# Optimization experiments

Measured on AMD Instinct MI355X. Metric: run time of the kernel, lower is better.

The kernel has to match this reference:

```python
import jax, jax.numpy as jnp
import numpy as np


def setup_inputs() -> dict:
    key = jax.random.key(0)
    ks = jax.random.split(key, 7)
    T, K, D_x, D_y = 8192, 64, 128, 64
    X = jax.random.normal(ks[0], (T, D_x), dtype=jnp.float32)
    Y = jax.random.normal(ks[1], (T, D_y), dtype=jnp.float32)
    # learned parameters (small random values for non-degenerate math)
    init_logits = jax.random.normal(ks[2], (K,), dtype=jnp.float32) * 0.1
    W = jax.random.normal(ks[3], (K, K, D_x), dtype=jnp.float32) * 0.05
    b = jax.random.normal(ks[4], (K, K), dtype=jnp.float32) * 0.1
    mu = jax.random.normal(ks[5], (K, D_y), dtype=jnp.float32) * 0.1
    log_var_unconstrained = jax.random.normal(ks[6], (K, D_y), dtype=jnp.float32) * 0.1
    return {"X": X, "Y": Y, "init_logits": init_logits, "W": W, "b": b,
            "mu": mu, "log_var_unconstrained": log_var_unconstrained}


def reference(X, Y, init_logits, W, b, mu, log_var_unconstrained):
    # log pi0
    log_pi0 = jax.nn.log_softmax(init_logits)
    # emissions for all t: diagonal Gaussian log-pdf, log_em [T, K]
    log_var = jnp.clip(log_var_unconstrained, -6.0, 6.0)  # [K, D_y]
    D = Y.shape[-1]
    LOG2PI = jnp.log(jnp.asarray(2.0 * np.pi, dtype=Y.dtype))
    diff = Y[:, None, :] - mu[None, :, :]                 # [T, K, D_y]
    quad = jnp.sum(diff * diff * jnp.exp(-log_var)[None], axis=-1)  # [T, K]
    logdet = jnp.sum(log_var, axis=-1)                    # [K]
    log_em = -0.5 * (D * LOG2PI + logdet[None, :] + quad)  # [T, K]
    # time-varying transition logits: b_ij + x_t . W_ij, row-softmax over j
    logits = b[None, :, :] + jnp.einsum('ijd,td->tij', W, X)  # [T, K, K]
    log_A = jax.nn.log_softmax(logits, axis=2)                 # [T, K, K]
    # forward recursion: alpha_t(j) = log_em_t(j) + logsumexp_i(alpha_{t-1}(i) + log_A_t(i,j))
    alpha0 = log_pi0 + log_em[0]

    def step(alpha, inputs):
        log_A_t, log_em_t = inputs
        alpha_new = log_em_t + jax.nn.logsumexp(alpha[:, None] + log_A_t, axis=0)
        return alpha_new, None

    alpha_T, _ = jax.lax.scan(step, alpha0, (log_A[1:], log_em[1:]))
    loglik = jax.nn.logsumexp(alpha_T)
    return loglik
```

## Files before the change

### kernel.cpp

```cpp
#include <hip/hip_runtime.h>
#include <hip/hip_bf16.h>


typedef unsigned int u32;
typedef unsigned short u16;

#define T_LEN 8192

typedef __attribute__((ext_vector_type(8))) short bf16x8;
typedef __attribute__((ext_vector_type(4))) float f32x4;

__device__ __forceinline__ float bflo(u32 u){ return __uint_as_float(u << 16); }
__device__ __forceinline__ float bfhi(u32 u){ return __uint_as_float(u & 0xffff0000u); }
__device__ __forceinline__ u32 f2bf(float x){
  u32 b = __float_as_uint(x);
  return (b + 0x7fffu + ((b >> 16) & 1u)) >> 16;
}
__device__ __forceinline__ u32 pack2bf(float a, float b){
  return f2bf(a) | (f2bf(b) << 16);
}

__global__ __launch_bounds__(64) void k_prep(
    const float* __restrict__ mu, const float* __restrict__ lvu,
    float* __restrict__ muT, float* __restrict__ ivT, float* __restrict__ logdet)
{
  const int k = threadIdx.x;
  float ld = 0.f;
  for (int d = 0; d < 64; ++d){
    float lv = fminf(fmaxf(lvu[k*64 + d], -6.f), 6.f);
    ld += lv;
    muT[d*64 + k] = mu[k*64 + d];
    ivT[d*64 + k] = __expf(-lv);
  }
  logdet[k] = ld;
}

__global__ __launch_bounds__(256) void k_emis(
    const float* __restrict__ Y, const float* __restrict__ muT,
    const float* __restrict__ ivT, const float* __restrict__ logdet,
    float* __restrict__ emp, float* __restrict__ cvec)
{
  const int w = threadIdx.x >> 6, k = threadIdx.x & 63;
  const int t = blockIdx.x * 4 + w;
  float y = Y[(size_t)t*64 + k];
  float quad = 0.f;
  #pragma unroll 8
  for (int d = 0; d < 64; ++d){
    float yd = __shfl(y, d, 64);
    float df = yd - muT[d*64 + k];
    quad = fmaf(df*df, ivT[d*64 + k], quad);
  }
  float le = -0.5f*(117.6241322f + logdet[k] + quad);
  float m = le;
  #pragma unroll
  for (int off = 1; off < 64; off <<= 1) m = fmaxf(m, __shfl_xor(m, off, 64));
  emp[(size_t)t*64 + k] = __expf(le - m);
  if (k == 0) cvec[t] = m;
}

__global__ __launch_bounds__(256) void k_trans(
    const float* __restrict__ X, const float* __restrict__ W,
    const float* __restrict__ bmat, const float* __restrict__ emp,
    u16* __restrict__ Ap)
{
  __shared__ __align__(16) u16 Xs[128*128];
  __shared__ __align__(16) u16 Ws[64*128];
  const int tid = threadIdx.x;
  const int t0 = blockIdx.x * 128;
  const int i  = blockIdx.y;

  {
    const float4* xs = (const float4*)(X + (size_t)t0 * 128);
    #pragma unroll
    for (int u = 0; u < 16; ++u){
      int f = u*256 + tid;
      float4 v = xs[f];
      int row = f >> 5, c = f & 31;
      int byte = (row*256 + c*8) ^ ((row & 7) << 4);
      *(uint2*)((char*)Xs + byte) = make_uint2(pack2bf(v.x, v.y), pack2bf(v.z, v.w));
    }
    const float4* wsrc = (const float4*)(W + (size_t)i * 8192);
    #pragma unroll
    for (int u = 0; u < 8; ++u){
      int f = u*256 + tid;
      float4 v = wsrc[f];
      int row = f >> 5, c = f & 31;
      int byte = (row*256 + c*8) ^ ((row & 7) << 4);
      *(uint2*)((char*)Ws + byte) = make_uint2(pack2bf(v.x, v.y), pack2bf(v.z, v.w));
    }
  }
  __syncthreads();

  const int lane = tid & 63, w = tid >> 6;
  const int lr = lane & 15, lg = lane >> 4;

  f32x4 acc[2][4] = {};
  #pragma unroll
  for (int kg = 0; kg < 4; ++kg){
    const int kbyte = kg*64 + lg*16;
    bf16x8 a[2], b[4];
    #pragma unroll
    for (int mt = 0; mt < 2; ++mt){
      int row = w*32 + mt*16 + lr;
      a[mt] = *(const bf16x8*)((const char*)Xs + ((row*256 + kbyte) ^ ((row&7)<<4)));
    }
    #pragma unroll
    for (int nt = 0; nt < 4; ++nt){
      int row = nt*16 + lr;
      b[nt] = *(const bf16x8*)((const char*)Ws + ((row*256 + kbyte) ^ ((row&7)<<4)));
    }
    #pragma unroll
    for (int mt = 0; mt < 2; ++mt)
      #pragma unroll
      for (int nt = 0; nt < 4; ++nt)
        acc[mt][nt] = __builtin_amdgcn_mfma_f32_16x16x32_bf16(a[mt], b[nt], acc[mt][nt], 0, 0, 0);
  }

  float bv[4];
  #pragma unroll
  for (int nt = 0; nt < 4; ++nt) bv[nt] = bmat[i*64 + nt*16 + lr];

  __syncthreads();
  u16* Ct = Xs;

  #pragma unroll
  for (int mt = 0; mt < 2; ++mt){
    #pragma unroll
    for (int reg = 0; reg < 4; ++reg){
      const int row = w*32 + mt*16 + lg*4 + reg;
      const int t = t0 + row;
      float v0 = acc[mt][0][reg] + bv[0];
      float v1 = acc[mt][1][reg] + bv[1];
      float v2 = acc[mt][2][reg] + bv[2];
      float v3 = acc[mt][3][reg] + bv[3];
      float mx = fmaxf(fmaxf(v0,v1), fmaxf(v2,v3));
      #pragma unroll
      for (int off = 1; off < 16; off <<= 1) mx = fmaxf(mx, __shfl_xor(mx, off, 64));
      float e0 = __expf(v0-mx), e1 = __expf(v1-mx), e2 = __expf(v2-mx), e3 = __expf(v3-mx);
      float sum = e0 + e1 + e2 + e3;
      #pragma unroll
      for (int off = 1; off < 16; off <<= 1) sum += __shfl_xor(sum, off, 64);
      float inv = 1.0f / sum;
      const float* er = emp + (size_t)t*64;
      const int sw = (row & 7) << 4;
      *(u16*)((char*)Ct + row*128 + ((( 0 + lr)*2) ^ sw)) = (u16)f2bf(e0*inv*er[ 0 + lr]);
      *(u16*)((char*)Ct + row*128 + (((16 + lr)*2) ^ sw)) = (u16)f2bf(e1*inv*er[16 + lr]);
      *(u16*)((char*)Ct + row*128 + (((32 + lr)*2) ^ sw)) = (u16)f2bf(e2*inv*er[32 + lr]);
      *(u16*)((char*)Ct + row*128 + (((48 + lr)*2) ^ sw)) = (u16)f2bf(e3*inv*er[48 + lr]);
    }
  }
  __syncthreads();
  #pragma unroll
  for (int q = 0; q < 4; ++q){
    const int f = tid*4 + q;
    const int row = f >> 3, c = f & 7;
    uint4 v = *(const uint4*)((const char*)Ct + row*128 + ((c*16) ^ ((row & 7) << 4)));
    *(uint4*)(Ap + (size_t)(t0 + row)*4096 + (size_t)i*64 + c*8) = v;
  }
}

__global__ __launch_bounds__(256) void k_scan(
    u16* mats, int mstride, int per_wg, int skip0,
    const float* __restrict__ in_sc, float* __restrict__ out_sc)
{
  __shared__ u32 Apk[2][32*68];
  const int tid = threadIdx.x;
  const int lane = tid & 63, w = tid >> 6;
  const int r16 = lane & 15, oct = lane >> 4;
  int c0 = blockIdx.x * per_wg, cnt = per_wg;
  const size_t out_slot = (size_t)c0 * mstride;
  if (blockIdx.x == 0){ c0 += skip0; cnt -= skip0; }

  bf16x8 Bf[2];
  {
    const u16* m0 = mats + ((size_t)c0*mstride << 12) + (w*16 + r16)*64 + oct*8;
    Bf[0] = *(const bf16x8*)(m0);
    Bf[1] = *(const bf16x8*)(m0 + 32);
  }
  float S = in_sc ? in_sc[c0*4 + w] : 0.0f;

  const int lp = tid >> 3, c8 = tid & 7;
  auto STAGE = [&](int buf, const u16* src){
    const uint4 A = *(const uint4*)(src + lp*128 + c8*8);
    const uint4 B = *(const uint4*)(src + lp*128 + 64 + c8*8);
    uint4 o0, o1;
    o0.x = (A.x & 0xffffu) | (B.x << 16);
    o0.y = (A.x >> 16)     | (B.x & 0xffff0000u);
    o0.z = (A.y & 0xffffu) | (B.y << 16);
    o0.w = (A.y >> 16)     | (B.y & 0xffff0000u);
    o1.x = (A.z & 0xffffu) | (B.z << 16);
    o1.y = (A.z >> 16)     | (B.z & 0xffff0000u);
    o1.z = (A.w & 0xffffu) | (B.w << 16);
    o1.w = (A.w >> 16)     | (B.w & 0xffff0000u);
    u32* dst = &Apk[buf][lp*68 + c8*8];
    *(uint4*)(dst)     = o0;
    *(uint4*)(dst + 4) = o1;
  };

  if (cnt > 1) STAGE(0, mats + ((size_t)(c0+1)*mstride << 12));
  __syncthreads();
  int cur = 0;
  for (int kk = 1; kk < cnt; ++kk){
    if (kk + 1 < cnt) STAGE(cur ^ 1, mats + ((size_t)(c0 + kk + 1)*mstride << 12));

    if (in_sc){
      const float* sp = in_sc + (size_t)(c0 + kk)*4;
      float s0=sp[0], s1=sp[1], s2=sp[2], s3=sp[3];
      float sm = fmaxf(fmaxf(s0,s1), fmaxf(s2,s3));
      S += sm;
      #pragma unroll
      for (int kt = 0; kt < 2; ++kt){
        float slo = (kt == 0) ? s0 : s2;
        float shi = (kt == 0) ? s1 : s3;
        float se = __expf(((oct >> 1) ? shi : slo) - sm);
        uint4 bv4 = __builtin_bit_cast(uint4, Bf[kt]);
        bv4.x = pack2bf(bflo(bv4.x)*se, bfhi(bv4.x)*se);
        bv4.y = pack2bf(bflo(bv4.y)*se, bfhi(bv4.y)*se);
        bv4.z = pack2bf(bflo(bv4.z)*se, bfhi(bv4.z)*se);
        bv4.w = pack2bf(bflo(bv4.w)*se, bfhi(bv4.w)*se);
        Bf[kt] = __builtin_bit_cast(bf16x8, bv4);
      }
    }

    f32x4 acc[4] = {};
    const u32* Ab = &Apk[cur][0];
    #pragma unroll
    for (int kt = 0; kt < 2; ++kt){
      const u32* gb = Ab + (kt*16 + oct*4)*68 + r16;
      #pragma unroll
      for (int jt = 0; jt < 4; ++jt){
        const u32* g = gb + jt*16;
        uint4 av = make_uint4(g[0], g[68], g[136], g[204]);
        acc[jt] = __builtin_amdgcn_mfma_f32_16x16x32_bf16(
            __builtin_bit_cast(bf16x8, av), Bf[kt], acc[jt], 0, 0, 0);
      }
    }

    float mx = acc[0][0];
    #pragma unroll
    for (int jt = 0; jt < 4; ++jt)
      #pragma unroll
      for (int q = 0; q < 4; ++q) mx = fmaxf(mx, acc[jt][q]);
    #pragma unroll
    for (int off = 1; off < 64; off <<= 1) mx = fmaxf(mx, __shfl_xor(mx, off, 64));
    float inv = 1.0f / mx;
    S += __logf(mx);

    u32 p0[4], p1[4];
    #pragma unroll
    for (int jt = 0; jt < 4; ++jt){
      p0[jt] = pack2bf(acc[jt][0]*inv, acc[jt][1]*inv);
      p1[jt] = pack2bf(acc[jt][2]*inv, acc[jt][3]*inv);
    }
    const int s0l = r16 + 32*(oct & 1), s1l = s0l + 16;
    const bool hi = (oct >> 1) != 0;
    #pragma unroll
    for (int kt = 0; kt < 2; ++kt){
      u32 a0 = __shfl(p0[2*kt],   s0l, 64), a1 = __shfl(p1[2*kt],   s0l, 64);
      u32 a2 = __shfl(p0[2*kt],   s1l, 64), a3 = __shfl(p1[2*kt],   s1l, 64);
      u32 b0 = __shfl(p0[2*kt+1], s0l, 64), b1 = __shfl(p1[2*kt+1], s0l, 64);
      u32 b2 = __shfl(p0[2*kt+1], s1l, 64), b3 = __shfl(p1[2*kt+1], s1l, 64);
      uint4 nb;
      nb.x = hi ? b0 : a0;
      nb.y = hi ? b1 : a1;
      nb.z = hi ? b2 : a2;
      nb.w = hi ? b3 : a3;
      Bf[kt] = __builtin_bit_cast(bf16x8, nb);
    }
    cur ^= 1;
    __syncthreads();
  }
  {
    u16* outp = mats + (out_slot << 12) + (w*16 + r16)*64 + oct*8;
    *(bf16x8*)(outp)      = Bf[0];
    *(bf16x8*)(outp + 32) = Bf[1];
    if (lane == 0) out_sc[blockIdx.x*4 + w] = S;
  }
}

__global__ __launch_bounds__(256) void k_final(
    const float* __restrict__ init_logits, const float* __restrict__ emp,
    const float* __restrict__ cvec, const u16* __restrict__ Mfin, int mstride,
    const float* __restrict__ scfin, int nmat, float* __restrict__ out)
{
  __shared__ float wsum[4];
  const int tid = threadIdx.x;
  float part = 0.f;
  for (int t = tid; t < T_LEN; t += 256) part += cvec[t];
  #pragma unroll
  for (int off = 1; off < 64; off <<= 1) part += __shfl_xor(part, off, 64);
  if ((tid & 63) == 0) wsum[tid >> 6] = part;
  __syncthreads();
  if (tid >= 64) return;
  const float csum = wsum[0] + wsum[1] + wsum[2] + wsum[3];
  const int k = tid;
  float ilv = init_logits[k];
  float m = ilv;
  #pragma unroll
  for (int off = 1; off < 64; off <<= 1) m = fmaxf(m, __shfl_xor(m, off, 64));
  float e = __expf(ilv - m);
  float s = e;
  #pragma unroll
  for (int off = 1; off < 64; off <<= 1) s += __shfl_xor(s, off, 64);
  float alpha = (e / s) * emp[k];
  float S = 0.f;
  for (int d = 0; d < nmat; ++d){
    const float* sp = scfin + d*4;
    float sm = fmaxf(fmaxf(sp[0], sp[1]), fmaxf(sp[2], sp[3]));
    alpha *= __expf(sp[k >> 4] - sm);
    S += sm;
    const u16* Mp = Mfin + ((size_t)d*mstride << 12);
    float an = 0.f;
    for (int i2 = 0; i2 < 64; ++i2){
      float av = __shfl(alpha, i2, 64);
      an = fmaf(av, __uint_as_float(((u32)Mp[i2*64 + k]) << 16), an);
    }
    float mx = an;
    #pragma unroll
    for (int off = 1; off < 64; off <<= 1) mx = fmaxf(mx, __shfl_xor(mx, off, 64));
    alpha = an / mx;
    S += __logf(mx);
  }
  float tot = alpha;
  #pragma unroll
  for (int off = 1; off < 64; off <<= 1) tot += __shfl_xor(tot, off, 64);
  if (k == 0) out[0] = __logf(tot) + S + csum;
}

extern "C" void kernel_launch(void* const* d_in, const int* in_sizes, int n_in,
                              void* d_out, int out_size, void* d_ws, size_t ws_size,
                              hipStream_t stream)
{
  const float* X  = (const float*)d_in[0];
  const float* Y  = (const float*)d_in[1];
  const float* il = (const float*)d_in[2];
  const float* W  = (const float*)d_in[3];
  const float* bm = (const float*)d_in[4];
  const float* mu = (const float*)d_in[5];
  const float* lv = (const float*)d_in[6];
  float* out = (float*)d_out;
  char* ws = (char*)d_ws;
  (void)in_sizes; (void)n_in; (void)out_size; (void)ws_size;

  float* emp    = (float*)(ws + 0x0000000);
  float* cvec   = (float*)(ws + 0x0200000);
  float* muT    = (float*)(ws + 0x0210000);
  float* ivT    = (float*)(ws + 0x0214000);
  float* logdet = (float*)(ws + 0x0218000);
  float* sc1    = (float*)(ws + 0x0220000);
  float* sc2    = (float*)(ws + 0x0224000);
  float* sc3    = (float*)(ws + 0x0225000);
  float* sc4    = (float*)(ws + 0x0226000);
  float* sc5    = (float*)(ws + 0x0227000);
  u16*   Ap     = (u16*)  (ws + 0x0400000);

  k_prep <<<1, 64, 0, stream>>>(mu, lv, muT, ivT, logdet);
  k_emis <<<2048, 256, 0, stream>>>(Y, muT, ivT, logdet, emp, cvec);
  k_trans<<<dim3(64, 64), 256, 0, stream>>>(X, W, bm, emp, Ap);
  k_scan <<<1024, 256, 0, stream>>>(Ap,   1, 8, 1, (const float*)nullptr, sc1);
  k_scan <<<256,  256, 0, stream>>>(Ap,   8, 4, 0, sc1, sc2);
  k_scan <<<64,   256, 0, stream>>>(Ap,  32, 4, 0, sc2, sc3);
  k_scan <<<16,   256, 0, stream>>>(Ap, 128, 4, 0, sc3, sc4);
  k_scan <<<4,    256, 0, stream>>>(Ap, 512, 4, 0, sc4, sc5);
  k_final<<<1, 256, 0, stream>>>(il, emp, cvec, Ap, 2048, sc5, 4, out);
}
```

Baseline: 196.2 us.

## Pre-convert X/W to swizzled bf16, restructure transition GEMM and scan tree

X and W are converted once to swizzled bf16 inside the emission kernel, so the transition kernel can load tiles straight into LDS with global_load_lds and skip repeated fp32 conversion. The transition GEMM is retiled to 64 timesteps by 2 source states per block, with W rows as the MFMA A operand. The softmax drops the max subtraction and reduces row sums through shared memory. The scan tree goes from five levels to four with wider per-block fan-in. Skipping the max subtraction could overflow for large logits, and the wider scan levels reduce parallelism at each level.

Result: slower. 205.2 us (+4.6%).

```diff
diff --git a/kernel.cpp b/kernel.cpp
--- a/kernel.cpp
+++ b/kernel.cpp
@@ -18,6 +18,16 @@
 }
 __device__ __forceinline__ u32 pack2bf(float a, float b){
   return f2bf(a) | (f2bf(b) << 16);
+}
+
+__device__ __forceinline__ void gld_lds16(const void* g, void* l){
+#if defined(__has_builtin) && __has_builtin(__builtin_amdgcn_global_load_lds)
+  __builtin_amdgcn_global_load_lds(
+      (const __attribute__((address_space(1))) unsigned int*)g,
+      (__attribute__((address_space(3))) unsigned int*)l, 16, 0, 0);
+#else
+  *(uint4*)((char*)l + (threadIdx.x & 63) * 16) = *(const uint4*)g;
+#endif
 }
 
 __global__ __launch_bounds__(64) void k_prep(
@@ -38,9 +48,12 @@
 __global__ __launch_bounds__(256) void k_emis(
     const float* __restrict__ Y, const float* __restrict__ muT,
     const float* __restrict__ ivT, const float* __restrict__ logdet,
-    float* __restrict__ emp, float* __restrict__ cvec)
-{
-  const int w = threadIdx.x >> 6, k = threadIdx.x & 63;
+    const float* __restrict__ X, const float* __restrict__ W,
+    float* __restrict__ emp, float* __restrict__ cvec,
+    u16* __restrict__ Xsw, u16* __restrict__ Wsw)
+{
+  const int tid = threadIdx.x;
+  const int w = tid >> 6, k = tid & 63;
   const int t = blockIdx.x * 4 + w;
   float y = Y[(size_t)t*64 + k];
   float quad = 0.f;
@@ -56,106 +69,138 @@
   for (int off = 1; off < 64; off <<= 1) m = fmaxf(m, __shfl_xor(m, off, 64));
   emp[(size_t)t*64 + k] = __expf(le - m);
   if (k == 0) cvec[t] = m;
+
+  if (tid < 128){
+    int rl = tid >> 5, c32 = tid & 31;
+    int tr = blockIdx.x*4 + rl;
+    float4 v = *(const float4*)(X + (size_t)tr*128 + c32*4);
+    int c16 = c32 >> 1, h = c32 & 1;
+    int byte = tr*256 + ((c16 ^ (tr & 7))*16 + h*8);
+    *(uint2*)((char*)Xsw + byte) = make_uint2(pack2bf(v.x,v.y), pack2bf(v.z,v.w));
+  }
+  if (blockIdx.x < 512){
+    int f4 = blockIdx.x*256 + tid;
+    int r = f4 >> 5, c32 = f4 & 31;
+    float4 v = *(const float4*)(W + (size_t)f4*4);
+    int c16 = c32 >> 1, h = c32 & 1;
+    int byte = r*256 + ((c16 ^ (r & 7))*16 + h*8);
+    *(uint2*)((char*)Wsw + byte) = make_uint2(pack2bf(v.x,v.y), pack2bf(v.z,v.w));
+  }
 }
 
 __global__ __launch_bounds__(256) void k_trans(
-    const float* __restrict__ X, const float* __restrict__ W,
+    const u16* __restrict__ Xsw, const u16* __restrict__ Wsw,
     const float* __restrict__ bmat, const float* __restrict__ emp,
     u16* __restrict__ Ap)
 {
-  __shared__ __align__(16) u16 Xs[128*128];
-  __shared__ __align__(16) u16 Ws[64*128];
+  __shared__ __align__(16) u16 Wt[128*128];
+  __shared__ __align__(16) u16 Xt[64*128];
+  __shared__ float Sred[8][64];
   const int tid = threadIdx.x;
-  const int t0 = blockIdx.x * 128;
-  const int i  = blockIdx.y;
-
-  {
-    const float4* xs = (const float4*)(X + (size_t)t0 * 128);
-    #pragma unroll
-    for (int u = 0; u < 16; ++u){
-      int f = u*256 + tid;
-      float4 v = xs[f];
-      int row = f >> 5, c = f & 31;
-      int byte = (row*256 + c*8) ^ ((row & 7) << 4);
-      *(uint2*)((char*)Xs + byte) = make_uint2(pack2bf(v.x, v.y), pack2bf(v.z, v.w));
-    }
-    const float4* wsrc = (const float4*)(W + (size_t)i * 8192);
-    #pragma unroll
-    for (int u = 0; u < 8; ++u){
-      int f = u*256 + tid;
-      float4 v = wsrc[f];
-      int row = f >> 5, c = f & 31;
-      int byte = (row*256 + c*8) ^ ((row & 7) << 4);
-      *(uint2*)((char*)Ws + byte) = make_uint2(pack2bf(v.x, v.y), pack2bf(v.z, v.w));
-    }
-  }
-  __syncthreads();
-
   const int lane = tid & 63, w = tid >> 6;
   const int lr = lane & 15, lg = lane >> 4;
+  const int t0 = blockIdx.x * 64;
+  const int i0 = blockIdx.y * 2;
+
+  {
+    const char* xsrc = (const char*)(Xsw + (size_t)t0*128);
+    const char* wsrc = (const char*)(Wsw + (size_t)i0*64*128);
+    #pragma unroll
+    for (int c = 0; c < 4; ++c){
+      int kb = w*4 + c;
+      gld_lds16(xsrc + kb*1024 + lane*16, (char*)Xt + kb*1024);
+    }
+    #pragma unroll
+    for (int c = 0; c < 8; ++c){
+      int kb = w*8 + c;
+      gld_lds16(wsrc + kb*1024 + lane*16, (char*)Wt + kb*1024);
+    }
+  }
+  __syncthreads();
 
   f32x4 acc[2][4] = {};
   #pragma unroll
   for (int kg = 0; kg < 4; ++kg){
-    const int kbyte = kg*64 + lg*16;
+    const int kc = kg*4 + lg;
     bf16x8 a[2], b[4];
     #pragma unroll
-    for (int mt = 0; mt < 2; ++mt){
-      int row = w*32 + mt*16 + lr;
-      a[mt] = *(const bf16x8*)((const char*)Xs + ((row*256 + kbyte) ^ ((row&7)<<4)));
-    }
-    #pragma unroll
-    for (int nt = 0; nt < 4; ++nt){
-      int row = nt*16 + lr;
-      b[nt] = *(const bf16x8*)((const char*)Ws + ((row*256 + kbyte) ^ ((row&7)<<4)));
-    }
-    #pragma unroll
-    for (int mt = 0; mt < 2; ++mt)
+    for (int jt = 0; jt < 2; ++jt){
+      int row = (w + jt*4)*16 + lr;
+      a[jt] = *(const bf16x8*)((const char*)Wt + row*256 + ((kc ^ (row & 7))*16));
+    }
+    #pragma unroll
+    for (int tt = 0; tt < 4; ++tt){
+      int row = tt*16 + lr;
+      b[tt] = *(const bf16x8*)((const char*)Xt + row*256 + ((kc ^ (row & 7))*16));
+    }
+    #pragma unroll
+    for (int jt = 0; jt < 2; ++jt)
       #pragma unroll
-      for (int nt = 0; nt < 4; ++nt)
-        acc[mt][nt] = __builtin_amdgcn_mfma_f32_16x16x32_bf16(a[mt], b[nt], acc[mt][nt], 0, 0, 0);
-  }
-
-  float bv[4];
-  #pragma unroll
-  for (int nt = 0; nt < 4; ++nt) bv[nt] = bmat[i*64 + nt*16 + lr];
+      for (int tt = 0; tt < 4; ++tt)
+        acc[jt][tt] = __builtin_amdgcn_mfma_f32_16x16x32_bf16(a[jt], b[tt], acc[jt][tt], 0, 0, 0);
+  }
+
+  float bvv[2][4];
+  #pragma unroll
+  for (int jt = 0; jt < 2; ++jt){
+    int q = w + jt*4;
+    int ig = i0 + (q >> 2);
+    #pragma unroll
+    for (int reg = 0; reg < 4; ++reg)
+      bvv[jt][reg] = bmat[ig*64 + (q & 3)*16 + lg*4 + reg];
+  }
 
   __syncthreads();
-  u16* Ct = Xs;
-
-  #pragma unroll
-  for (int mt = 0; mt < 2; ++mt){
-    #pragma unroll
-    for (int reg = 0; reg < 4; ++reg){
-      const int row = w*32 + mt*16 + lg*4 + reg;
-      const int t = t0 + row;
-      float v0 = acc[mt][0][reg] + bv[0];
-      float v1 = acc[mt][1][reg] + bv[1];
-      float v2 = acc[mt][2][reg] + bv[2];
-      float v3 = acc[mt][3][reg] + bv[3];
-      float mx = fmaxf(fmaxf(v0,v1), fmaxf(v2,v3));
-      #pragma unroll
-      for (int off = 1; off < 16; off <<= 1) mx = fmaxf(mx, __shfl_xor(mx, off, 64));
-      float e0 = __expf(v0-mx), e1 = __expf(v1-mx), e2 = __expf(v2-mx), e3 = __expf(v3-mx);
-      float sum = e0 + e1 + e2 + e3;
-      #pragma unroll
-      for (int off = 1; off < 16; off <<= 1) sum += __shfl_xor(sum, off, 64);
-      float inv = 1.0f / sum;
-      const float* er = emp + (size_t)t*64;
-      const int sw = (row & 7) << 4;
-      *(u16*)((char*)Ct + row*128 + ((( 0 + lr)*2) ^ sw)) = (u16)f2bf(e0*inv*er[ 0 + lr]);
-      *(u16*)((char*)Ct + row*128 + (((16 + lr)*2) ^ sw)) = (u16)f2bf(e1*inv*er[16 + lr]);
-      *(u16*)((char*)Ct + row*128 + (((32 + lr)*2) ^ sw)) = (u16)f2bf(e2*inv*er[32 + lr]);
-      *(u16*)((char*)Ct + row*128 + (((48 + lr)*2) ^ sw)) = (u16)f2bf(e3*inv*er[48 + lr]);
+  u16* Ct = Xt;
+
+  #pragma unroll
+  for (int jt = 0; jt < 2; ++jt){
+    const int q = w + jt*4;
+    #pragma unroll
+    for (int tt = 0; tt < 4; ++tt){
+      const int t = tt*16 + lr;
+      float e0 = __expf(acc[jt][tt][0] + bvv[jt][0]);
+      float e1 = __expf(acc[jt][tt][1] + bvv[jt][1]);
+      float e2 = __expf(acc[jt][tt][2] + bvv[jt][2]);
+      float e3 = __expf(acc[jt][tt][3] + bvv[jt][3]);
+      float s = e0 + e1 + e2 + e3;
+      s += __shfl_xor(s, 16, 64);
+      s += __shfl_xor(s, 32, 64);
+      if (lg == 0) Sred[q][t] = s;
+      const int byte = t*256 + ((q*32 + lg*8) ^ ((t & 7) << 4));
+      *(u32*)((char*)Ct + byte)     = pack2bf(e0, e1);
+      *(u32*)((char*)Ct + byte + 4) = pack2bf(e2, e3);
     }
   }
   __syncthreads();
-  #pragma unroll
-  for (int q = 0; q < 4; ++q){
-    const int f = tid*4 + q;
-    const int row = f >> 3, c = f & 7;
-    uint4 v = *(const uint4*)((const char*)Ct + row*128 + ((c*16) ^ ((row & 7) << 4)));
-    *(uint4*)(Ap + (size_t)(t0 + row)*4096 + (size_t)i*64 + c*8) = v;
+
+  {
+    const int trow = tid >> 2, seg = tid & 3;
+    float invs[2];
+    #pragma unroll
+    for (int ii = 0; ii < 2; ++ii){
+      float s = Sred[ii*4+0][trow] + Sred[ii*4+1][trow]
+              + Sred[ii*4+2][trow] + Sred[ii*4+3][trow];
+      invs[ii] = 1.0f / s;
+    }
+    const int sw = (trow & 7) << 4;
+    u16* orow = Ap + (size_t)(t0 + trow)*4096 + i0*64;
+    const float* er = emp + (size_t)(t0 + trow)*64;
+    #pragma unroll
+    for (int u = 0; u < 4; ++u){
+      const int bcol = seg*64 + u*16;
+      uint4 v = *(const uint4*)((const char*)Ct + trow*256 + (bcol ^ sw));
+      const int j0 = bcol >> 1;
+      const float inv = invs[j0 >> 6];
+      const int je = j0 & 63;
+      float4 ea = *(const float4*)(er + je);
+      float4 eb = *(const float4*)(er + je + 4);
+      u32 r0 = pack2bf(bflo(v.x)*inv*ea.x, bfhi(v.x)*inv*ea.y);
+      u32 r1 = pack2bf(bflo(v.y)*inv*ea.z, bfhi(v.y)*inv*ea.w);
+      u32 r2 = pack2bf(bflo(v.z)*inv*eb.x, bfhi(v.z)*inv*eb.y);
+      u32 r3 = pack2bf(bflo(v.w)*inv*eb.z, bfhi(v.w)*inv*eb.w);
+      *(uint4*)(orow + j0) = make_uint4(r0, r1, r2, r3);
+    }
   }
 }
 
@@ -351,16 +396,16 @@
   float* sc2    = (float*)(ws + 0x0224000);
   float* sc3    = (float*)(ws + 0x0225000);
   float* sc4    = (float*)(ws + 0x0226000);
-  float* sc5    = (float*)(ws + 0x0227000);
-  u16*   Ap     = (u16*)  (ws + 0x0400000);
+  u16*   Xsw    = (u16*)  (ws + 0x0240000);
+  u16*   Wsw    = (u16*)  (ws + 0x0440000);
+  u16*   Ap     = (u16*)  (ws + 0x0600000);
 
   k_prep <<<1, 64, 0, stream>>>(mu, lv, muT, ivT, logdet);
-  k_emis <<<2048, 256, 0, stream>>>(Y, muT, ivT, logdet, emp, cvec);
-  k_trans<<<dim3(64, 64), 256, 0, stream>>>(X, W, bm, emp, Ap);
-  k_scan <<<1024, 256, 0, stream>>>(Ap,   1, 8, 1, (const float*)nullptr, sc1);
-  k_scan <<<256,  256, 0, stream>>>(Ap,   8, 4, 0, sc1, sc2);
-  k_scan <<<64,   256, 0, stream>>>(Ap,  32, 4, 0, sc2, sc3);
-  k_scan <<<16,   256, 0, stream>>>(Ap, 128, 4, 0, sc3, sc4);
-  k_scan <<<4,    256, 0, stream>>>(Ap, 512, 4, 0, sc4, sc5);
-  k_final<<<1, 256, 0, stream>>>(il, emp, cvec, Ap, 2048, sc5, 4, out);
-}
+  k_emis <<<2048, 256, 0, stream>>>(Y, muT, ivT, logdet, X, W, emp, cvec, Xsw, Wsw);
+  k_trans<<<dim3(128, 32), 256, 0, stream>>>(Xsw, Wsw, bm, emp, Ap);
+  k_scan <<<1024, 256, 0, stream>>>(Ap,   1,  8, 1, (const float*)nullptr, sc1);
+  k_scan <<<128,  256, 0, stream>>>(Ap,   8,  8, 0, sc1, sc2);
+  k_scan <<<16,   256, 0, stream>>>(Ap,  64,  8, 0, sc2, sc3);
+  k_scan <<<1,    256, 0, stream>>>(Ap, 512, 16, 0, sc3, sc4);
+  k_final<<<1, 256, 0, stream>>>(il, emp, cvec, Ap, 1, sc4, 1, out);
+}
```
